# Optimization experiments

Hardware: AMD Instinct MI355X
Metric: run time of the kernel (lower is better)

## Reference

```python
import jax, jax.numpy as jnp
import numpy as np

N_HEAD = 16

def _rope_cos_sin(T, head_dim, dtype):
    # inv_freq over even indices, freqs [T, head_dim//2]
    inv_freq = 1.0 / (10000.0 ** (jnp.arange(0, head_dim, 2, dtype=jnp.float32) / head_dim))
    t = jnp.arange(T, dtype=jnp.float32)
    freqs = t[:, None] * inv_freq[None, :]
    cos = jnp.cos(freqs).astype(dtype)[None, :, None, :]  # [1,T,1,hd/2]
    sin = jnp.sin(freqs).astype(dtype)[None, :, None, :]
    return cos, sin

def _apply_rope(x, cos, sin):
    # x: [B,T,H,hd]; interleaved halves as in the torch module
    x1, x2 = x[..., ::2], x[..., 1::2]
    return jnp.concatenate([x1 * cos - x2 * sin, x1 * sin + x2 * cos], axis=-1)

def setup_inputs() -> dict:
    key = jax.random.key(0)
    k1, k2, k3 = jax.random.split(key, 3)
    B, T, C = 2, 2048, 1024
    x = jax.random.normal(k1, (B, T, C), dtype=jnp.float32)
    # causal mask (mask==0 positions get -inf), broadcast over B and heads
    attn_mask = jnp.tril(jnp.ones((T, T), dtype=bool))[None, None, :, :]
    w_qkv = jax.random.normal(k2, (C, 3 * C), dtype=jnp.float32) * (1.0 / np.sqrt(C))
    w_out = jax.random.normal(k3, (C, C), dtype=jnp.float32) * (1.0 / np.sqrt(C))
    return {"x": x, "attn_mask": attn_mask, "w_qkv": w_qkv, "w_out": w_out}

def reference(x, attn_mask, w_qkv, w_out):
    B, T, C = x.shape
    H = N_HEAD
    hd = C // H
    qkv = x @ w_qkv  # [B,T,3C]
    q, k, v = jnp.split(qkv, 3, axis=2)
    q = q.reshape(B, T, H, hd)
    k = k.reshape(B, T, H, hd)
    v = v.reshape(B, T, H, hd)
    cos, sin = _rope_cos_sin(T, hd, x.dtype)
    q = _apply_rope(q, cos, sin)
    k = _apply_rope(k, cos, sin)
    scale = 1.0 / np.sqrt(hd).astype(np.float32)
    att = jnp.einsum('bthd,bshd->bhts', q, k) * scale  # [B,H,T,T]
    att = jnp.where(attn_mask, att, -jnp.inf)
    att = jax.nn.softmax(att, axis=-1)
    out = jnp.einsum('bhts,bshd->bthd', att, v).reshape(B, T, C)
    out = out @ w_out
    k_t = jnp.transpose(k, (0, 2, 1, 3))  # [B,H,T,hd]
    v_t = jnp.transpose(v, (0, 2, 1, 3))
    return out, k_t, v_t
```

## Files before the change

kernel.cpp:

```cpp
#include <hip/hip_runtime.h>

#define T_SEQ 2048
#define NH    16
#define HD    64
#define CDIM  1024
#define BDIM  2

using floatx4 = __attribute__((ext_vector_type(4))) float;
using bf16x8  = __attribute__((ext_vector_type(8))) __bf16;
using half4   = __attribute__((ext_vector_type(4))) _Float16;
using half8   = __attribute__((ext_vector_type(8))) _Float16;
typedef unsigned short u16;

__device__ __forceinline__ u16 f2bf(float f) {
  unsigned int u = __float_as_uint(f);
  u += 0x7fffu + ((u >> 16) & 1u);
  return (u16)(u >> 16);
}
__device__ __forceinline__ float bf2f(u16 h) {
  return __uint_as_float(((unsigned int)h) << 16);
}
__device__ __forceinline__ u16 f2h(float f) {
  union { _Float16 h; u16 u; } c; c.h = (_Float16)f; return c.u;
}
__device__ __forceinline__ unsigned pk2h(float a, float b) {
  return __builtin_bit_cast(unsigned, __builtin_amdgcn_cvt_pkrtz(a, b));
}
__device__ __forceinline__ void gld16(const void* g, const void* l) {
  __builtin_amdgcn_global_load_lds(
      (const __attribute__((address_space(1))) unsigned int*)(unsigned long long)g,
      (__attribute__((address_space(3))) unsigned int*)(unsigned int)(unsigned long long)l,
      16, 0, 0);
}

__global__ __launch_bounds__(256) void preproc(const float* __restrict__ x,
                                               const float* __restrict__ w_qkv,
                                               const float* __restrict__ w_out,
                                               u16* __restrict__ xb,
                                               u16* __restrict__ wqT,
                                               u16* __restrict__ woT) {
  __shared__ float tile[32][33];
  int blk = blockIdx.x, tid = threadIdx.x;
  if (blk < 4096) {
    int i = blk * 256 + tid;
    float4 v = ((const float4*)x)[i];
    ushort4 o;
    o.x = f2bf(v.x); o.y = f2bf(v.y); o.z = f2bf(v.z); o.w = f2bf(v.w);
    ((ushort4*)xb)[i] = o;
    return;
  }
  const float* W; u16* WT; int K, N, bx, by;
  if (blk < 4096 + 3072) {
    int idx = blk - 4096; W = w_qkv; WT = wqT; K = 1024; N = 3072;
    bx = idx % 96; by = idx / 96;
  } else {
    int idx = blk - 7168; W = w_out; WT = woT; K = 1024; N = 1024;
    bx = idx & 31; by = idx >> 5;
  }
  int n0 = bx * 32, k0 = by * 32;
  int tx = tid & 31, ty = tid >> 5;
#pragma unroll
  for (int i = 0; i < 32; i += 8)
    tile[ty + i][tx] = W[(size_t)(k0 + ty + i) * N + n0 + tx];
  __syncthreads();
#pragma unroll
  for (int i = 0; i < 32; i += 8)
    WT[(size_t)(n0 + ty + i) * K + k0 + tx] = f2bf(tile[tx][ty + i]);
}

template <bool OUT_F32>
__global__ __launch_bounds__(256) void gemm_bt(const u16* __restrict__ A,
                                               const u16* __restrict__ BT,
                                               float* __restrict__ Cf,
                                               u16* __restrict__ Cb,
                                               int M, int N, int K) {
  __shared__ u16 As[2][128 * 32];
  __shared__ u16 Bs[2][128 * 32];
  const int tid  = threadIdx.x;
  const int lane = tid & 63, wave = tid >> 6;
  const int quad = lane >> 4, l16 = lane & 15;
  const int wm = (wave & 1) * 64, wn = (wave >> 1) * 64;
  const int bid = blockIdx.y * gridDim.x + blockIdx.x;
  const int cpx = (gridDim.x * gridDim.y) >> 3;
  const int swz = (bid & 7) * cpx + (bid >> 3);
  const int row0 = (swz & 31) * 128, col0 = (swz >> 5) * 128;
  const int srow = tid >> 2;
  const int sc   = tid & 3;
  const int sgc  = (sc ^ ((srow >> 1) & 3)) * 8;
  floatx4 acc[4][4] = {};

  auto stage = [&](int buf, int k0) {
    gld16(A  + (size_t)(row0 + srow     ) * K + k0 + sgc, &As[buf][srow * 32 + sc * 8]);
    gld16(A  + (size_t)(row0 + srow + 64) * K + k0 + sgc, &As[buf][(srow + 64) * 32 + sc * 8]);
    gld16(BT + (size_t)(col0 + srow     ) * K + k0 + sgc, &Bs[buf][srow * 32 + sc * 8]);
    gld16(BT + (size_t)(col0 + srow + 64) * K + k0 + sgc, &Bs[buf][(srow + 64) * 32 + sc * 8]);
  };

  const int nk = K >> 5;
  stage(0, 0);
  for (int ki = 0; ki < nk; ki++) {
    const int cur = ki & 1;
    __builtin_amdgcn_s_barrier();
    int kn = ki + 1 < nk ? ki + 1 : nk - 1;
    stage(cur ^ 1, kn << 5);
    asm volatile("s_waitcnt vmcnt(4)" ::: "memory");
    __builtin_amdgcn_s_barrier();
    bf16x8 af[4], bfv[4];
#pragma unroll
    for (int mt = 0; mt < 4; mt++) {
      int r = wm + mt * 16 + l16;
      af[mt] = *(const bf16x8*)&As[cur][r * 32 + (quad ^ ((r >> 1) & 3)) * 8];
    }
#pragma unroll
    for (int nt = 0; nt < 4; nt++) {
      int r = wn + nt * 16 + l16;
      bfv[nt] = *(const bf16x8*)&Bs[cur][r * 32 + (quad ^ ((r >> 1) & 3)) * 8];
    }
#pragma unroll
    for (int mt = 0; mt < 4; mt++)
#pragma unroll
      for (int nt = 0; nt < 4; nt++)
        acc[mt][nt] = __builtin_amdgcn_mfma_f32_16x16x32_bf16(af[mt], bfv[nt], acc[mt][nt], 0, 0, 0);
  }
  asm volatile("s_waitcnt vmcnt(0)" ::: "memory");
#pragma unroll
  for (int mt = 0; mt < 4; mt++)
#pragma unroll
    for (int nt = 0; nt < 4; nt++)
#pragma unroll
      for (int r = 0; r < 4; r++) {
        int row = row0 + wm + mt * 16 + quad * 4 + r;
        int col = col0 + wn + nt * 16 + l16;
        float v = acc[mt][nt][r];
        if (OUT_F32) Cf[(size_t)row * N + col] = v;
        else         Cb[(size_t)row * N + col] = f2bf(v);
      }
}

__global__ __launch_bounds__(256) void rope_vpack(const u16* __restrict__ qkv,
                                                  u16* __restrict__ qf16,
                                                  u16* __restrict__ kf16,
                                                  float* __restrict__ kt_out,
                                                  float* __restrict__ vt_out,
                                                  u16* __restrict__ vtf) {
  int blk = blockIdx.x;
  if (blk < 8192) {
    int rowid = blk * 8 + (threadIdx.x >> 5);
    int p     = threadIdx.x & 31;
    int t     = rowid & (T_SEQ - 1);
    int h     = (rowid >> 11) & 15;
    int b     = rowid >> 15;
    const u16* qrow = qkv + ((size_t)(b * T_SEQ + t)) * 3072 + h * 64;
    unsigned int qp = *(const unsigned int*)(qrow + 2 * p);
    unsigned int kp = *(const unsigned int*)(qrow + 1024 + 2 * p);
    float q1 = bf2f((u16)qp), q2 = bf2f((u16)(qp >> 16));
    float k1 = bf2f((u16)kp), k2 = bf2f((u16)(kp >> 16));
    float inv_rev = exp2f(-0.4152410118609203f * (float)p) * 0.15915494309189535f;
    float rev = (float)t * inv_rev;
    float fr  = rev - floorf(rev);
    float sn = __builtin_amdgcn_sinf(fr);
    float cs = __builtin_amdgcn_cosf(fr);
    float qv1 = q1 * cs - q2 * sn, qv2 = q1 * sn + q2 * cs;
    float kv1 = k1 * cs - k2 * sn, kv2 = k1 * sn + k2 * cs;
    size_t o = (size_t)rowid * 64;
    const float s = 0.18033688011112042f;
    qf16[o + p]      = f2h(qv1 * s);
    qf16[o + p + 32] = f2h(qv2 * s);
    kf16[o + p]      = f2h(kv1);
    kf16[o + p + 32] = f2h(kv2);
    kt_out[o + p]      = kv1;
    kt_out[o + p + 32] = kv2;
    return;
  }
  __shared__ float tile[64][65];
  int b2 = blk - 8192;
  int t0 = (b2 & 31) * 64;
  int bh = b2 >> 5;
  int b = bh >> 4, h = bh & 15;
  int tx = threadIdx.x & 63, ty = threadIdx.x >> 6;
#pragma unroll
  for (int i = ty; i < 64; i += 4) {
    float v = bf2f(qkv[((size_t)(b * T_SEQ + t0 + i)) * 3072 + 2048 + h * 64 + tx]);
    tile[i][tx] = v;
    vt_out[((size_t)bh * T_SEQ + t0 + i) * 64 + tx] = v;
  }
  __syncthreads();
#pragma unroll
  for (int i = ty; i < 64; i += 4)
    vtf[((size_t)bh * 64 + i) * T_SEQ + t0 + tx] = f2h(tile[tx][i]);
}

__device__ __forceinline__ void qk_dual(const u16* Ks, const half8* qfA, const half8* qfB,
                                        floatx4 (&sA)[8], floatx4 (&sB)[8],
                                        int quad, int l16) {
#pragma unroll
  for (int kc = 0; kc < 2; kc++)
#pragma unroll
    for (int st = 0; st < 8; st++) {
      int srow = st * 16 + l16;
      half8 ak = *(const half8*)&Ks[srow * 64 + (((kc * 4 + quad) ^ (srow & 7)) * 8)];
      sA[st] = __builtin_amdgcn_mfma_f32_16x16x32_f16(ak, qfA[kc], sA[st], 0, 0, 0);
      sB[st] = __builtin_amdgcn_mfma_f32_16x16x32_f16(ak, qfB[kc], sB[st], 0, 0, 0);
    }
}
__device__ __forceinline__ void qk_single(const u16* Ks, const half8* qfA,
                                          floatx4 (&sA)[8], int quad, int l16) {
#pragma unroll
  for (int kc = 0; kc < 2; kc++)
#pragma unroll
    for (int st = 0; st < 8; st++) {
      int srow = st * 16 + l16;
      half8 ak = *(const half8*)&Ks[srow * 64 + (((kc * 4 + quad) ^ (srow & 7)) * 8)];
      sA[st] = __builtin_amdgcn_mfma_f32_16x16x32_f16(ak, qfA[kc], sA[st], 0, 0, 0);
    }
}
__device__ __forceinline__ void apply_mask(floatx4 (&s)[8], int kt, int tw, int quad, int l16) {
  int tg = tw + l16;
#pragma unroll
  for (int st = 0; st < 8; st++) {
    int sg = kt * 128 + st * 16 + quad * 4;
#pragma unroll
    for (int r = 0; r < 4; r++)
      if (sg + r > tg) s[st][r] = -1e30f;
  }
}
__device__ __forceinline__ float vmax4(const floatx4& v) {
  return fmaxf(fmaxf(fmaxf(v[0], v[1]), v[2]), v[3]);
}
__device__ __forceinline__ void softmax_update(floatx4 (&s)[8], float& mrow,
                                               floatx4& lsum, floatx4 (&oacc)[4]) {
  float p0 = fmaxf(vmax4(s[0]), vmax4(s[1]));
  float p1 = fmaxf(vmax4(s[2]), vmax4(s[3]));
  float p2 = fmaxf(vmax4(s[4]), vmax4(s[5]));
  float p3 = fmaxf(vmax4(s[6]), vmax4(s[7]));
  float mx = fmaxf(fmaxf(fmaxf(p0, p1), p2), p3);
  mx = fmaxf(mx, __shfl_xor(mx, 16));
  mx = fmaxf(mx, __shfl_xor(mx, 32));
  if (!__all(mx <= mrow + 8.f)) {
    float mnew = fmaxf(mrow, mx);
    float alpha = exp2f(mrow - mnew);
    mrow = mnew;
    lsum *= alpha;
#pragma unroll
    for (int dt = 0; dt < 4; dt++) oacc[dt] *= alpha;
  }
#pragma unroll
  for (int st = 0; st < 8; st++)
#pragma unroll
    for (int r = 0; r < 4; r++) s[st][r] = exp2f(s[st][r] - mrow);
}
__device__ __forceinline__ void pv_dual(const u16* Vts, const floatx4 (&sA)[8],
                                        const floatx4 (&sB)[8], floatx4 (&oA)[4],
                                        floatx4 (&oB)[4], floatx4& lsA, floatx4& lsB,
                                        int qh2, int ql2, int l16) {
  const half4 vones = {(_Float16)1.f, (_Float16)1.f, (_Float16)1.f, (_Float16)1.f};
#pragma unroll
  for (int st = 0; st < 8; st++) {
    union { unsigned u[2]; half4 h; } pa, pb;
    pa.u[0] = pk2h(sA[st][0], sA[st][1]); pa.u[1] = pk2h(sA[st][2], sA[st][3]);
    pb.u[0] = pk2h(sB[st][0], sB[st][1]); pb.u[1] = pk2h(sB[st][2], sB[st][3]);
    lsA = __builtin_amdgcn_mfma_f32_16x16x16f16(vones, pa.h, lsA, 0, 0, 0);
    lsB = __builtin_amdgcn_mfma_f32_16x16x16f16(vones, pb.h, lsB, 0, 0, 0);
#pragma unroll
    for (int dt = 0; dt < 4; dt++) {
      int drow = dt * 16 + l16;
      half4 av = *(const half4*)&Vts[drow * 128 + (((st * 2 + qh2) ^ (drow & 15)) * 8) + ql2];
      oA[dt] = __builtin_amdgcn_mfma_f32_16x16x16f16(av, pa.h, oA[dt], 0, 0, 0);
      oB[dt] = __builtin_amdgcn_mfma_f32_16x16x16f16(av, pb.h, oB[dt], 0, 0, 0);
    }
  }
}
__device__ __forceinline__ void pv_single(const u16* Vts, const floatx4 (&sA)[8],
                                          floatx4 (&oA)[4], floatx4& lsA,
                                          int qh2, int ql2, int l16) {
  const half4 vones = {(_Float16)1.f, (_Float16)1.f, (_Float16)1.f, (_Float16)1.f};
#pragma unroll
  for (int st = 0; st < 8; st++) {
    union { unsigned u[2]; half4 h; } pa;
    pa.u[0] = pk2h(sA[st][0], sA[st][1]); pa.u[1] = pk2h(sA[st][2], sA[st][3]);
    lsA = __builtin_amdgcn_mfma_f32_16x16x16f16(vones, pa.h, lsA, 0, 0, 0);
#pragma unroll
    for (int dt = 0; dt < 4; dt++) {
      int drow = dt * 16 + l16;
      half4 av = *(const half4*)&Vts[drow * 128 + (((st * 2 + qh2) ^ (drow & 15)) * 8) + ql2];
      oA[dt] = __builtin_amdgcn_mfma_f32_16x16x16f16(av, pa.h, oA[dt], 0, 0, 0);
    }
  }
}
__device__ __forceinline__ void epilogue(u16* __restrict__ Ob, const floatx4 (&oacc)[4],
                                         const floatx4& lsum, int b, int h, int tw,
                                         int quad, int l16) {
  int t = tw + l16;
  float invl = 1.f / lsum[0];
#pragma unroll
  for (int dt = 0; dt < 4; dt++) {
    int d0 = dt * 16 + quad * 4;
    ushort4 o;
    o.x = f2bf(oacc[dt][0] * invl);
    o.y = f2bf(oacc[dt][1] * invl);
    o.z = f2bf(oacc[dt][2] * invl);
    o.w = f2bf(oacc[dt][3] * invl);
    *(ushort4*)&Ob[((size_t)(b * T_SEQ) + t) * CDIM + h * HD + d0] = o;
  }
}

__global__ __launch_bounds__(256, 2) void attn_fused(const u16* __restrict__ qf16,
                                                     const u16* __restrict__ kf16,
                                                     const u16* __restrict__ vtf,
                                                     u16* __restrict__ Ob) {
  __shared__ u16 Ks[128 * 64];
  __shared__ u16 Vts[64 * 128];
  const int tid = threadIdx.x;
  const int lane = tid & 63, wave = tid >> 6;
  const int quad = lane >> 4, l16 = lane & 15;
  const int qh2 = quad >> 1, ql2 = (quad & 1) * 4;
  const int j   = blockIdx.x >> 5;
  const int bh  = blockIdx.x & 31;
  const int b = bh >> 4, h = bh & 15;

  const int qtA = 31 - j, qtB = j;
  const int twA = qtA * 64 + wave * 16;
  const int twB = qtB * 64 + wave * 16;
  const int nktA = (qtA >> 1) + 1;
  const int nktB = (qtB >> 1) + 1;

  const u16* QgA = qf16 + ((size_t)bh * T_SEQ + twA) * HD;
  const u16* QgB = qf16 + ((size_t)bh * T_SEQ + twB) * HD;
  half8 qfA[2], qfB[2];
#pragma unroll
  for (int kc = 0; kc < 2; kc++) {
    qfA[kc] = *(const half8*)&QgA[(size_t)l16 * HD + kc * 32 + quad * 8];
    qfB[kc] = *(const half8*)&QgB[(size_t)l16 * HD + kc * 32 + quad * 8];
  }

  floatx4 oaccA[4] = {}, oaccB[4] = {};
  floatx4 lsA = {}, lsB = {};
  float mA = -1e30f, mB = -1e30f;

#pragma unroll 1
  for (int kt = 0; kt < nktA; kt++) {
    __syncthreads();
    const size_t koff = ((size_t)bh * T_SEQ + kt * 128) * HD;
    const u16* Vg = vtf + (size_t)bh * HD * T_SEQ + kt * 128;
#pragma unroll
    for (int jj = 0; jj < 4; jj++) {
      int t2 = jj * 256 + tid;
      int r = t2 >> 3, c = t2 & 7;
      gld16(kf16 + koff + r * HD + (c ^ (r & 7)) * 8, &Ks[t2 * 8]);
    }
#pragma unroll
    for (int jj = 0; jj < 4; jj++) {
      int t2 = jj * 256 + tid;
      int r = t2 >> 4, c = t2 & 15;
      gld16(Vg + (size_t)r * T_SEQ + (c ^ (r & 15)) * 8, &Vts[t2 * 8]);
    }
    __syncthreads();

    if (kt < nktB) {
      floatx4 sA[8] = {}, sB[8] = {};
      qk_dual(Ks, qfA, qfB, sA, sB, quad, l16);
      if (kt == nktB - 1) apply_mask(sB, kt, twB, quad, l16);
      softmax_update(sA, mA, lsA, oaccA);
      softmax_update(sB, mB, lsB, oaccB);
      pv_dual(Vts, sA, sB, oaccA, oaccB, lsA, lsB, qh2, ql2, l16);
    } else {
      floatx4 sA[8] = {};
      qk_single(Ks, qfA, sA, quad, l16);
      if (kt == nktA - 1) apply_mask(sA, kt, twA, quad, l16);
      softmax_update(sA, mA, lsA, oaccA);
      pv_single(Vts, sA, oaccA, lsA, qh2, ql2, l16);
    }
  }
  epilogue(Ob, oaccA, lsA, b, h, twA, quad, l16);
  epilogue(Ob, oaccB, lsB, b, h, twB, quad, l16);
}

extern "C" void kernel_launch(void* const* d_in, const int* in_sizes, int n_in,
                              void* d_out, int out_size, void* d_ws, size_t ws_size,
                              hipStream_t stream) {
  const float* x     = (const float*)d_in[0];
  const float* w_qkv = (const float*)d_in[2];
  const float* w_out = (const float*)d_in[3];
  float* out    = (float*)d_out;
  float* kt_out = out + (size_t)BDIM * T_SEQ * CDIM;
  float* vt_out = kt_out + (size_t)BDIM * T_SEQ * CDIM;

  const size_t F = (size_t)4194304;
  char* base = (char*)d_ws;
  u16* xb   = (u16*)base;
  u16* wqT  = xb + F;
  u16* woT  = wqT + (size_t)3145728;
  u16* qkvb = woT + (size_t)1048576;
  u16* qf16 = qkvb + (size_t)3 * F;
  u16* kf16 = qf16 + F;
  u16* vtf  = (u16*)base;
  u16* Ob   = kf16 + F;

  preproc<<<8192, 256, 0, stream>>>(x, w_qkv, w_out, xb, wqT, woT);
  gemm_bt<false><<<dim3(32, 24), 256, 0, stream>>>(xb, wqT, (float*)nullptr, qkvb, 4096, 3072, 1024);
  rope_vpack<<<9216, 256, 0, stream>>>(qkvb, qf16, kf16, kt_out, vt_out, vtf);
  attn_fused<<<512, 256, 0, stream>>>(qf16, kf16, vtf, Ob);
  gemm_bt<true><<<dim3(32, 8), 256, 0, stream>>>(Ob, woT, out, (u16*)nullptr, 4096, 1024, 1024);
}
```

Before: 207.3 us.

## Fuse RoPE and V transpose into QKV GEMM epilogue with permuted weight columns

The separate rope_vpack kernel is removed. Its work now runs in the epilogue of a dedicated QKV GEMM: the Q/K weight columns are permuted during preprocessing so that each thread holds both interleaved RoPE halves, and a precomputed cos/sin table is built in extra preproc blocks. V is written in fp32 directly and transposed to fp16 through LDS. This avoids writing the bf16 qkv buffer and reading it back in another launch. The costs are more scattered epilogue stores and table lookups inside the GEMM.

```diff
diff --git a/kernel.cpp b/kernel.cpp
--- a/kernel.cpp
+++ b/kernel.cpp
@@ -38,9 +38,19 @@
                                                const float* __restrict__ w_out,
                                                u16* __restrict__ xb,
                                                u16* __restrict__ wqT,
-                                               u16* __restrict__ woT) {
+                                               u16* __restrict__ woT,
+                                               float2* __restrict__ tab) {
   __shared__ float tile[32][33];
   int blk = blockIdx.x, tid = threadIdx.x;
+  if (blk >= 8192) {
+    int idx = (blk - 8192) * 256 + tid;
+    int t = idx >> 5, i = idx & 31;
+    float inv_rev = exp2f(-0.4152410118609203f * (float)i) * 0.15915494309189535f;
+    float rev = (float)t * inv_rev;
+    float fr  = rev - floorf(rev);
+    tab[idx] = make_float2(__builtin_amdgcn_cosf(fr), __builtin_amdgcn_sinf(fr));
+    return;
+  }
   if (blk < 4096) {
     int i = blk * 256 + tid;
     float4 v = ((const float4*)x)[i];
@@ -64,8 +74,141 @@
     tile[ty + i][tx] = W[(size_t)(k0 + ty + i) * N + n0 + tx];
   __syncthreads();
 #pragma unroll
-  for (int i = 0; i < 32; i += 8)
-    WT[(size_t)(n0 + ty + i) * K + k0 + tx] = f2bf(tile[tx][ty + i]);
+  for (int i = 0; i < 32; i += 8) {
+    int n = n0 + ty + i;
+    int dest = n;
+    if (N == 3072 && n < 2048) {
+      int f = n & 63;
+      dest = (n & ~63) | ((f >> 1) + ((f & 1) << 5));
+    }
+    WT[(size_t)dest * K + k0 + tx] = f2bf(tile[tx][ty + i]);
+  }
+}
+
+__global__ __launch_bounds__(256) void gemm_qkv_fused(const u16* __restrict__ A,
+                                                      const u16* __restrict__ BT,
+                                                      const float2* __restrict__ tab,
+                                                      u16* __restrict__ qf16,
+                                                      u16* __restrict__ kf16,
+                                                      float* __restrict__ kt_out,
+                                                      float* __restrict__ vt_out,
+                                                      u16* __restrict__ vtf) {
+  __shared__ u16 smem[4][128 * 32];
+  const int K = 1024;
+  const int tid  = threadIdx.x;
+  const int lane = tid & 63, wave = tid >> 6;
+  const int quad = lane >> 4, l16 = lane & 15;
+  const int wm = (wave & 1) * 64, wn = (wave >> 1) * 64;
+  const int bid = blockIdx.y * gridDim.x + blockIdx.x;
+  const int cpx = (gridDim.x * gridDim.y) >> 3;
+  const int swz = (bid & 7) * cpx + (bid >> 3);
+  const int row0 = (swz & 31) * 128, col0 = (swz >> 5) * 128;
+  const int srow = tid >> 2;
+  const int sc   = tid & 3;
+  const int sgc  = (sc ^ ((srow >> 1) & 3)) * 8;
+  floatx4 acc[4][4] = {};
+
+  auto stage = [&](int buf, int k0) {
+    gld16(A  + (size_t)(row0 + srow     ) * K + k0 + sgc, &smem[buf][srow * 32 + sc * 8]);
+    gld16(A  + (size_t)(row0 + srow + 64) * K + k0 + sgc, &smem[buf][(srow + 64) * 32 + sc * 8]);
+    gld16(BT + (size_t)(col0 + srow     ) * K + k0 + sgc, &smem[2 + buf][srow * 32 + sc * 8]);
+    gld16(BT + (size_t)(col0 + srow + 64) * K + k0 + sgc, &smem[2 + buf][(srow + 64) * 32 + sc * 8]);
+  };
+
+  const int nk = K >> 5;
+  stage(0, 0);
+  for (int ki = 0; ki < nk; ki++) {
+    const int cur = ki & 1;
+    __builtin_amdgcn_s_barrier();
+    int kn = ki + 1 < nk ? ki + 1 : nk - 1;
+    stage(cur ^ 1, kn << 5);
+    asm volatile("s_waitcnt vmcnt(4)" ::: "memory");
+    __builtin_amdgcn_s_barrier();
+    bf16x8 af[4], bfv[4];
+#pragma unroll
+    for (int mt = 0; mt < 4; mt++) {
+      int r = wm + mt * 16 + l16;
+      af[mt] = *(const bf16x8*)&smem[cur][r * 32 + (quad ^ ((r >> 1) & 3)) * 8];
+    }
+#pragma unroll
+    for (int nt = 0; nt < 4; nt++) {
+      int r = wn + nt * 16 + l16;
+      bfv[nt] = *(const bf16x8*)&smem[2 + cur][r * 32 + (quad ^ ((r >> 1) & 3)) * 8];
+    }
+#pragma unroll
+    for (int mt = 0; mt < 4; mt++)
+#pragma unroll
+      for (int nt = 0; nt < 4; nt++)
+        acc[mt][nt] = __builtin_amdgcn_mfma_f32_16x16x32_bf16(af[mt], bfv[nt], acc[mt][nt], 0, 0, 0);
+  }
+  asm volatile("s_waitcnt vmcnt(0)" ::: "memory");
+
+  const int sec = col0 >> 10;
+  const int h   = ((col0 & 1023) + wn) >> 6;
+  const int b   = row0 >> 11;
+  const int tbase = (row0 & 2047) + wm;
+  const size_t hb = (size_t)(b * NH + h) * T_SEQ;
+
+  if (sec < 2) {
+    const float S = 0.18033688011112042f;
+#pragma unroll
+    for (int mt = 0; mt < 4; mt++)
+#pragma unroll
+      for (int r = 0; r < 4; r++) {
+        int t = tbase + mt * 16 + quad * 4 + r;
+        size_t rb = (hb + t) * 64;
+#pragma unroll
+        for (int no = 0; no < 2; no++) {
+          int i = no * 16 + l16;
+          float2 cn = tab[t * 32 + i];
+          float x1 = acc[mt][no][r], x2 = acc[mt][no + 2][r];
+          float o1 = x1 * cn.x - x2 * cn.y;
+          float o2 = x1 * cn.y + x2 * cn.x;
+          if (sec == 0) {
+            qf16[rb + i]      = f2h(o1 * S);
+            qf16[rb + i + 32] = f2h(o2 * S);
+          } else {
+            kf16[rb + i]      = f2h(o1);
+            kf16[rb + i + 32] = f2h(o2);
+            kt_out[rb + i]      = o1;
+            kt_out[rb + i + 32] = o2;
+          }
+        }
+      }
+  } else {
+#pragma unroll
+    for (int mt = 0; mt < 4; mt++)
+#pragma unroll
+      for (int nt = 0; nt < 4; nt++)
+#pragma unroll
+        for (int r = 0; r < 4; r++) {
+          int t = tbase + mt * 16 + quad * 4 + r;
+          vt_out[(hb + t) * 64 + nt * 16 + l16] = acc[mt][nt][r];
+        }
+    __syncthreads();
+    u16* tb = &smem[0][0] + wave * 2432;
+#pragma unroll
+    for (int p = 0; p < 2; p++) {
+#pragma unroll
+      for (int mt = 0; mt < 4; mt++)
+#pragma unroll
+        for (int ntl = 0; ntl < 2; ntl++)
+#pragma unroll
+          for (int r = 0; r < 4; r++) {
+            int dl = ntl * 16 + l16;
+            int rowr = mt * 16 + quad * 4 + r;
+            tb[dl * 72 + rowr] = f2h(acc[mt][p * 2 + ntl][r]);
+          }
+#pragma unroll
+      for (int it = 0; it < 8; it++) {
+        int dl = it * 4 + quad;
+        int d  = p * 32 + dl;
+        ushort4 vv = *(const ushort4*)&tb[dl * 72 + l16 * 4];
+        *(ushort4*)&vtf[((size_t)(b * NH + h) * 64 + d) * T_SEQ + tbase + l16 * 4] = vv;
+      }
+      __syncthreads();
+    }
+  }
 }
 
 template <bool OUT_F32>
@@ -137,59 +280,6 @@
       }
 }
 
-__global__ __launch_bounds__(256) void rope_vpack(const u16* __restrict__ qkv,
-                                                  u16* __restrict__ qf16,
-                                                  u16* __restrict__ kf16,
-                                                  float* __restrict__ kt_out,
-                                                  float* __restrict__ vt_out,
-                                                  u16* __restrict__ vtf) {
-  int blk = blockIdx.x;
-  if (blk < 8192) {
-    int rowid = blk * 8 + (threadIdx.x >> 5);
-    int p     = threadIdx.x & 31;
-    int t     = rowid & (T_SEQ - 1);
-    int h     = (rowid >> 11) & 15;
-    int b     = rowid >> 15;
-    const u16* qrow = qkv + ((size_t)(b * T_SEQ + t)) * 3072 + h * 64;
-    unsigned int qp = *(const unsigned int*)(qrow + 2 * p);
-    unsigned int kp = *(const unsigned int*)(qrow + 1024 + 2 * p);
-    float q1 = bf2f((u16)qp), q2 = bf2f((u16)(qp >> 16));
-    float k1 = bf2f((u16)kp), k2 = bf2f((u16)(kp >> 16));
-    float inv_rev = exp2f(-0.4152410118609203f * (float)p) * 0.15915494309189535f;
-    float rev = (float)t * inv_rev;
-    float fr  = rev - floorf(rev);
-    float sn = __builtin_amdgcn_sinf(fr);
-    float cs = __builtin_amdgcn_cosf(fr);
-    float qv1 = q1 * cs - q2 * sn, qv2 = q1 * sn + q2 * cs;
-    float kv1 = k1 * cs - k2 * sn, kv2 = k1 * sn + k2 * cs;
-    size_t o = (size_t)rowid * 64;
-    const float s = 0.18033688011112042f;
-    qf16[o + p]      = f2h(qv1 * s);
-    qf16[o + p + 32] = f2h(qv2 * s);
-    kf16[o + p]      = f2h(kv1);
-    kf16[o + p + 32] = f2h(kv2);
-    kt_out[o + p]      = kv1;
-    kt_out[o + p + 32] = kv2;
-    return;
-  }
-  __shared__ float tile[64][65];
-  int b2 = blk - 8192;
-  int t0 = (b2 & 31) * 64;
-  int bh = b2 >> 5;
-  int b = bh >> 4, h = bh & 15;
-  int tx = threadIdx.x & 63, ty = threadIdx.x >> 6;
-#pragma unroll
-  for (int i = ty; i < 64; i += 4) {
-    float v = bf2f(qkv[((size_t)(b * T_SEQ + t0 + i)) * 3072 + 2048 + h * 64 + tx]);
-    tile[i][tx] = v;
-    vt_out[((size_t)bh * T_SEQ + t0 + i) * 64 + tx] = v;
-  }
-  __syncthreads();
-#pragma unroll
-  for (int i = ty; i < 64; i += 4)
-    vtf[((size_t)bh * 64 + i) * T_SEQ + t0 + tx] = f2h(tile[tx][i]);
-}
-
 __device__ __forceinline__ void qk_dual(const u16* Ks, const half8* qfA, const half8* qfB,
                                         floatx4 (&sA)[8], floatx4 (&sB)[8],
                                         int quad, int l16) {
@@ -390,15 +480,14 @@
   u16* xb   = (u16*)base;
   u16* wqT  = xb + F;
   u16* woT  = wqT + (size_t)3145728;
-  u16* qkvb = woT + (size_t)1048576;
-  u16* qf16 = qkvb + (size_t)3 * F;
+  u16* qf16 = woT + (size_t)1048576;
   u16* kf16 = qf16 + F;
-  u16* vtf  = (u16*)base;
-  u16* Ob   = kf16 + F;
-
-  preproc<<<8192, 256, 0, stream>>>(x, w_qkv, w_out, xb, wqT, woT);
-  gemm_bt<false><<<dim3(32, 24), 256, 0, stream>>>(xb, wqT, (float*)nullptr, qkvb, 4096, 3072, 1024);
-  rope_vpack<<<9216, 256, 0, stream>>>(qkvb, qf16, kf16, kt_out, vt_out, vtf);
+  u16* vtf  = kf16 + F;
+  u16* Ob   = vtf + F;
+  float2* tab = (float2*)(base + (size_t)48 * 1024 * 1024);
+
+  preproc<<<8448, 256, 0, stream>>>(x, w_qkv, w_out, xb, wqT, woT, tab);
+  gemm_qkv_fused<<<dim3(32, 24), 256, 0, stream>>>(xb, wqT, tab, qf16, kf16, kt_out, vt_out, vtf);
   attn_fused<<<512, 256, 0, stream>>>(qf16, kf16, vtf, Ob);
   gemm_bt<true><<<dim3(32, 8), 256, 0, stream>>>(Ob, woT, out, (u16*)nullptr, 4096, 1024, 1024);
 }
```

New measurement: 202.2 us. 2.5% less time.
